# Kernel tuning notes

Measured on AMD Instinct MI355X. Metric: run time of the kernel, lower is better.

## Reference

```python
import jax, jax.numpy as jnp
import numpy as np
import math

D = 1024
H = 16
B = 4
S = 2048


def setup_inputs() -> dict:
    key = jax.random.key(0)
    ks = jax.random.split(key, 11)
    s = 1.0 / math.sqrt(D)
    inp = {
        "queries": jax.random.normal(ks[0], (B, S, D), jnp.float32),
        "keys": jax.random.normal(ks[1], (B, S, D), jnp.float32),
        "values": jax.random.normal(ks[2], (B, S, D), jnp.float32),
        "Wq": jax.random.normal(ks[3], (D, D), jnp.float32) * s,
        "bq": jnp.zeros((D,), jnp.float32),
        "Wk": jax.random.normal(ks[4], (D, D), jnp.float32) * s,
        "bk": jnp.zeros((D,), jnp.float32),
        "Wv": jax.random.normal(ks[5], (D, D), jnp.float32) * s,
        "bv": jnp.zeros((D,), jnp.float32),
        "Wo": jax.random.normal(ks[6], (D, D), jnp.float32) * s,
        "bo": jnp.zeros((D,), jnp.float32),
    }
    return inp


def _split_heads(x):
    # [B, S, D] -> [B, H, S, D//H]
    b, s, d = x.shape
    return x.reshape(b, s, H, d // H).transpose(0, 2, 1, 3)


def reference(queries, keys, values, Wq, bq, Wk, bk, Wv, bv, Wo, bo):
    q = jax.nn.relu(queries @ Wq + bq)
    k = jax.nn.relu(keys @ Wk + bk)
    v = jax.nn.relu(values @ Wv + bv)
    q, k, v = _split_heads(q), _split_heads(k), _split_heads(v)
    dk = q.shape[-1]
    scores = jnp.einsum('bhqd,bhkd->bhqk', q, k) / jnp.sqrt(jnp.float32(dk))
    attn = jax.nn.softmax(scores, axis=-1)
    y = jnp.einsum('bhqk,bhkd->bhqd', attn, v)
    y = y.transpose(0, 2, 1, 3).reshape(queries.shape[0], queries.shape[1], -1)
    return jax.nn.relu(y @ Wo + bo)
```

## Files before the change

### kernel.cpp

```cpp
#include <hip/hip_runtime.h>
#include <hip/hip_bf16.h>
#include <stdint.h>

#define D_MODEL 1024
#define NH 16
#define BB 4
#define SS 2048
#define DKH 64
#define MTOT (BB*SS)

typedef float  f32x4  __attribute__((ext_vector_type(4)));
typedef short  bf16x8 __attribute__((ext_vector_type(8)));
typedef short  bf16x4 __attribute__((ext_vector_type(4)));

static __device__ __forceinline__ unsigned short f2bf(float x) {
    __hip_bfloat16 h = __float2bfloat16(x);
    return *reinterpret_cast<unsigned short*>(&h);
}

static __device__ __forceinline__ void gld_lds16(const void* g, void* l) {
    __builtin_amdgcn_global_load_lds(
        (__attribute__((address_space(1))) const void*)g,
        (__attribute__((address_space(3))) void*)l,
        16, 0, 0);
}

__global__ void cvt_f32_bf16(const float* __restrict__ in,
                             unsigned short* __restrict__ out) {
    const size_t i = ((size_t)blockIdx.x * blockDim.x + threadIdx.x) * 8;
    f32x4 a = *(const f32x4*)(in + i);
    f32x4 b = *(const f32x4*)(in + i + 4);
    bf16x8 o;
#pragma unroll
    for (int j = 0; j < 4; ++j) o[j] = (short)f2bf(a[j]);
#pragma unroll
    for (int j = 0; j < 4; ++j) o[4 + j] = (short)f2bf(b[j]);
    *(bf16x8*)(out + i) = o;
}

__global__ void transpose_cvt(const float* __restrict__ W,
                              unsigned short* __restrict__ WT) {
    __shared__ float tile[32][33];
    const int tx = threadIdx.x;
    const int ty = threadIdx.y;
    const int n0 = blockIdx.x * 32;
    const int k0 = blockIdx.y * 32;
#pragma unroll
    for (int i = 0; i < 32; i += 8)
        tile[ty + i][tx] = W[(size_t)(k0 + ty + i) * D_MODEL + n0 + tx];
    __syncthreads();
#pragma unroll
    for (int i = 0; i < 32; i += 8)
        WT[(size_t)(n0 + ty + i) * D_MODEL + k0 + tx] = f2bf(tile[tx][ty + i]);
}

__global__ __launch_bounds__(256)
void transpose_v(const unsigned short* __restrict__ Vh,
                 unsigned short* __restrict__ Vt) {
    __shared__ unsigned short t[64 * 64];
    const int tid = threadIdx.x;
    const int bh = blockIdx.y;
    const int s0 = blockIdx.x * 64;
    const unsigned short* src = Vh + ((size_t)bh * SS + s0) * DKH;
#pragma unroll
    for (int i = 0; i < 2; ++i) {
        const int v = tid + i * 256;
        const int r = v >> 3;
        const int c = (v & 7) * 8;
        bf16x8 x = *(const bf16x8*)&src[r * DKH + c];
#pragma unroll
        for (int j = 0; j < 8; ++j) {
            const int d = c + j;
            t[d * 64 + (r ^ ((d & 7) << 3))] = (unsigned short)x[j];
        }
    }
    __syncthreads();
    unsigned short* dst = Vt + (size_t)bh * DKH * SS + s0;
#pragma unroll
    for (int i = 0; i < 2; ++i) {
        const int v = tid + i * 256;
        const int d = v >> 3;
        const int ch = (v & 7) * 8;
        bf16x8 o = *(const bf16x8*)&t[d * 64 + ch];
        *(bf16x8*)&dst[(size_t)d * SS + ch] = o;
    }
}

template<int OUT_MODE>
__global__ __launch_bounds__(256)
void gemm_bt_bias_relu(const unsigned short* __restrict__ A,
                       const unsigned short* __restrict__ BT,
                       const float* __restrict__ bias,
                       void* __restrict__ out, float oscale) {
    constexpr int K = 1024, N = 1024, BM = 128, BN = 128, BK = 32;
    __shared__ __align__(16) unsigned short As[BM * BK];
    __shared__ __align__(16) unsigned short Bs[BN * BK];
    const int tid = threadIdx.x;
    const int lane = tid & 63;
    const int w = tid >> 6;
    const int wr = w >> 1, wc = w & 1;
    const int row16 = lane & 15, quad = lane >> 4;
    const int bm = blockIdx.x, bn = blockIdx.y;

    const unsigned short* Ab = A + (size_t)bm * BM * K;
    const unsigned short* Bb = BT + (size_t)bn * BN * K;

    f32x4 acc[4][4] = {};

    for (int k0 = 0; k0 < K; k0 += BK) {
        __syncthreads();
#pragma unroll
        for (int i = 0; i < 2; ++i) {
            const int o = tid * 8 + i * 2048;
            const int r = o >> 5, c = o & 31;
            gld_lds16(Ab + (size_t)r * K + k0 + c, As + o);
            gld_lds16(Bb + (size_t)r * K + k0 + c, Bs + o);
        }
        __syncthreads();
        bf16x8 af[4], bfr[4];
#pragma unroll
        for (int m = 0; m < 4; ++m)
            af[m] = *(const bf16x8*)&As[(wr * 64 + m * 16 + row16) * BK + quad * 8];
#pragma unroll
        for (int n = 0; n < 4; ++n)
            bfr[n] = *(const bf16x8*)&Bs[(wc * 64 + n * 16 + row16) * BK + quad * 8];
        __builtin_amdgcn_s_setprio(1);
#pragma unroll
        for (int m = 0; m < 4; ++m)
#pragma unroll
            for (int n = 0; n < 4; ++n)
                acc[m][n] = __builtin_amdgcn_mfma_f32_16x16x32_bf16(af[m], bfr[n], acc[m][n], 0, 0, 0);
        __builtin_amdgcn_s_setprio(0);
    }

#pragma unroll
    for (int m = 0; m < 4; ++m) {
#pragma unroll
        for (int n = 0; n < 4; ++n) {
            const int gcol = bn * BN + wc * 64 + n * 16 + row16;
            const float bv = bias[gcol];
#pragma unroll
            for (int r = 0; r < 4; ++r) {
                const int grow = bm * BM + wr * 64 + m * 16 + quad * 4 + r;
                float v = fmaxf((acc[m][n][r] + bv) * oscale, 0.0f);
                if (OUT_MODE == 0) {
                    const int b = grow >> 11, s = grow & (SS - 1);
                    const int h = gcol >> 6, d = gcol & (DKH - 1);
                    ((unsigned short*)out)[(((size_t)(b * NH + h) * SS + s) * DKH) + d] = f2bf(v);
                } else {
                    ((float*)out)[(size_t)grow * N + gcol] = v;
                }
            }
        }
    }
}

__global__ __launch_bounds__(256)
void flash_attn(const unsigned short* __restrict__ Qh,
                const unsigned short* __restrict__ Kh,
                const unsigned short* __restrict__ Vt,
                unsigned short* __restrict__ Y) {
    constexpr int KVB = 64;
    __shared__ __align__(16) unsigned short Ks[2 * KVB * 32];
    __shared__ __align__(16) unsigned short Vs[DKH * 64];
    __shared__ __align__(16) unsigned short Ps[4][16 * 64];

    const int tid = threadIdx.x;
    const int lane = tid & 63;
    const int w = tid >> 6;
    const int row16 = lane & 15, quad = lane >> 4;
    const int bh = blockIdx.y;
    const int q0 = blockIdx.x * 64;
    const size_t ho = (size_t)bh * SS * DKH;
    const unsigned short* Qp = Qh + ho;
    const unsigned short* Kp = Kh + ho;
    const unsigned short* Vtp = Vt + ho;
    unsigned short* Pw = &Ps[w][0];

    const int qrow = q0 + w * 16 + row16;
    const bf16x8 qf0 = *(const bf16x8*)&Qp[(size_t)qrow * DKH + quad * 8];
    const bf16x8 qf1 = *(const bf16x8*)&Qp[(size_t)qrow * DKH + 32 + quad * 8];

    const int sw = (row16 & 7) << 3;
    const int xsw0 = (quad * 8) ^ sw;
    const int xsw1 = (32 + quad * 8) ^ sw;

    float m_run[4], l_run[4];
    f32x4 yacc[4] = {};
#pragma unroll
    for (int r = 0; r < 4; ++r) { m_run[r] = -1e30f; l_run[r] = 0.0f; }

    for (int t = 0; t < SS / KVB; ++t) {
        const unsigned short* Kt = Kp + (size_t)t * KVB * DKH;
        __syncthreads();
#pragma unroll
        for (int i = 0; i < 2; ++i) {
            const int o = tid * 8 + i * 2048;
            const int c = o >> 11, rem = o & 2047;
            const int key = rem >> 5, kk = rem & 31;
            gld_lds16(Kt + (size_t)key * DKH + c * 32 + kk, Ks + o);
        }
#pragma unroll
        for (int i = 0; i < 2; ++i) {
            const int c = tid + i * 256;
            const int d = c >> 3, x = (c & 7) * 8;
            gld_lds16(Vtp + (size_t)d * SS + t * KVB + x, Vs + c * 8);
        }
        __syncthreads();

        f32x4 sc[4];
        __builtin_amdgcn_s_setprio(1);
#pragma unroll
        for (int kt = 0; kt < 4; ++kt) {
            bf16x8 kf0 = *(const bf16x8*)&Ks[(kt * 16 + row16) * 32 + quad * 8];
            bf16x8 kf1 = *(const bf16x8*)&Ks[2048 + (kt * 16 + row16) * 32 + quad * 8];
            f32x4 z = {};
            z = __builtin_amdgcn_mfma_f32_16x16x32_bf16(qf0, kf0, z, 0, 0, 0);
            z = __builtin_amdgcn_mfma_f32_16x16x32_bf16(qf1, kf1, z, 0, 0, 0);
            sc[kt] = z;
        }
        __builtin_amdgcn_s_setprio(0);

        float pmax[4];
#pragma unroll
        for (int r = 0; r < 4; ++r) {
            float mx = fmaxf(fmaxf(sc[0][r], sc[1][r]), fmaxf(sc[2][r], sc[3][r]));
#pragma unroll
            for (int off = 1; off < 16; off <<= 1)
                mx = fmaxf(mx, __shfl_xor(mx, off));
            pmax[r] = mx;
        }
        int need = 0;
#pragma unroll
        for (int r = 0; r < 4; ++r) need |= (pmax[r] > m_run[r] + 8.0f);
        if (__any(need)) {
#pragma unroll
            for (int r = 0; r < 4; ++r) {
                const float mnew = fmaxf(m_run[r], pmax[r]);
                const float corr = __builtin_amdgcn_exp2f(m_run[r] - mnew);
                m_run[r] = mnew;
                l_run[r] *= corr;
#pragma unroll
                for (int dt = 0; dt < 4; ++dt) yacc[dt][r] *= corr;
            }
        }
#pragma unroll
        for (int kt = 0; kt < 4; ++kt) {
#pragma unroll
            for (int r = 0; r < 4; ++r) {
                const float p = __builtin_amdgcn_exp2f(sc[kt][r] - m_run[r]);
                l_run[r] += p;
                const int row = quad * 4 + r;
                Pw[row * 64 + ((kt * 16 + row16) ^ ((row & 7) << 3))] = f2bf(p);
            }
        }
        {
            bf16x8 pf0 = *(const bf16x8*)&Pw[row16 * 64 + xsw0];
            bf16x8 pf1 = *(const bf16x8*)&Pw[row16 * 64 + xsw1];
            __builtin_amdgcn_s_setprio(1);
#pragma unroll
            for (int dt = 0; dt < 4; ++dt) {
                bf16x8 vf0 = *(const bf16x8*)&Vs[(dt * 16 + row16) * 64 + xsw0];
                yacc[dt] = __builtin_amdgcn_mfma_f32_16x16x32_bf16(pf0, vf0, yacc[dt], 0, 0, 0);
            }
#pragma unroll
            for (int dt = 0; dt < 4; ++dt) {
                bf16x8 vf1 = *(const bf16x8*)&Vs[(dt * 16 + row16) * 64 + xsw1];
                yacc[dt] = __builtin_amdgcn_mfma_f32_16x16x32_bf16(pf1, vf1, yacc[dt], 0, 0, 0);
            }
            __builtin_amdgcn_s_setprio(0);
        }
    }

    float inv[4];
#pragma unroll
    for (int r = 0; r < 4; ++r) {
        float s = l_run[r];
#pragma unroll
        for (int off = 1; off < 16; off <<= 1)
            s += __shfl_xor(s, off);
        inv[r] = 1.0f / s;
    }
    const int b = bh >> 4, h = bh & 15;
#pragma unroll
    for (int dt = 0; dt < 4; ++dt) {
#pragma unroll
        for (int r = 0; r < 4; ++r) {
            const int row = q0 + w * 16 + quad * 4 + r;
            const int col = h * DKH + dt * 16 + row16;
            Y[(size_t)(b * SS + row) * D_MODEL + col] = f2bf(yacc[dt][r] * inv[r]);
        }
    }
}

extern "C" void kernel_launch(void* const* d_in, const int* in_sizes, int n_in,
                              void* d_out, int out_size, void* d_ws, size_t ws_size,
                              hipStream_t stream) {
    (void)in_sizes; (void)n_in; (void)out_size; (void)ws_size;
    const float* queries = (const float*)d_in[0];
    const float* keys    = (const float*)d_in[1];
    const float* values  = (const float*)d_in[2];
    const float* Wq = (const float*)d_in[3];
    const float* bq = (const float*)d_in[4];
    const float* Wk = (const float*)d_in[5];
    const float* bk = (const float*)d_in[6];
    const float* Wv = (const float*)d_in[7];
    const float* bv = (const float*)d_in[8];
    const float* Wo = (const float*)d_in[9];
    const float* bo = (const float*)d_in[10];

    unsigned short* ws = (unsigned short*)d_ws;
    const size_t SZX = (size_t)MTOT * D_MODEL;
    const size_t SZW = (size_t)D_MODEL * D_MODEL;
    unsigned short* Xq  = ws;
    unsigned short* Xk  = ws + SZX;
    unsigned short* Xv  = ws + 2 * SZX;
    unsigned short* WqT = ws + 3 * SZX;
    unsigned short* WkT = WqT + SZW;
    unsigned short* WvT = WkT + SZW;
    unsigned short* WoT = WvT + SZW;
    unsigned short* Qh  = WoT + SZW;
    unsigned short* Kh  = Qh + SZX;
    unsigned short* Vh  = Kh + SZX;
    unsigned short* Vtr = Xv;
    unsigned short* Yb  = Xq;

    dim3 cblk(256), cgrid((unsigned)(SZX / (256 * 8)));
    cvt_f32_bf16<<<cgrid, cblk, 0, stream>>>(queries, Xq);
    cvt_f32_bf16<<<cgrid, cblk, 0, stream>>>(keys, Xk);
    cvt_f32_bf16<<<cgrid, cblk, 0, stream>>>(values, Xv);

    dim3 tgrid(32, 32), tblk(32, 8);
    transpose_cvt<<<tgrid, tblk, 0, stream>>>(Wq, WqT);
    transpose_cvt<<<tgrid, tblk, 0, stream>>>(Wk, WkT);
    transpose_cvt<<<tgrid, tblk, 0, stream>>>(Wv, WvT);
    transpose_cvt<<<tgrid, tblk, 0, stream>>>(Wo, WoT);

    const float qscale = 0.125f * 1.4426950408889634f;
    dim3 ggrid(MTOT / 128, D_MODEL / 128), gblk(256);
    gemm_bt_bias_relu<0><<<ggrid, gblk, 0, stream>>>(Xq, WqT, bq, Qh, qscale);
    gemm_bt_bias_relu<0><<<ggrid, gblk, 0, stream>>>(Xk, WkT, bk, Kh, 1.0f);
    gemm_bt_bias_relu<0><<<ggrid, gblk, 0, stream>>>(Xv, WvT, bv, Vh, 1.0f);

    dim3 vtgrid(SS / 64, BB * NH);
    transpose_v<<<vtgrid, gblk, 0, stream>>>(Vh, Vtr);

    dim3 agrid(SS / 64, BB * NH), ablk(256);
    flash_attn<<<agrid, ablk, 0, stream>>>(Qh, Kh, Vtr, Yb);

    gemm_bt_bias_relu<1><<<ggrid, gblk, 0, stream>>>(Yb, WoT, bo, d_out, 1.0f);
}
```

Measured before the change: 466.0 us.

## Double-buffer GEMM and attention LDS tiles, merge conversion launches, cheapen rescale check

```diff
diff --git a/kernel.cpp b/kernel.cpp
--- a/kernel.cpp
+++ b/kernel.cpp
@@ -11,7 +11,6 @@
 
 typedef float  f32x4  __attribute__((ext_vector_type(4)));
 typedef short  bf16x8 __attribute__((ext_vector_type(8)));
-typedef short  bf16x4 __attribute__((ext_vector_type(4)));
 
 static __device__ __forceinline__ unsigned short f2bf(float x) {
     __hip_bfloat16 h = __float2bfloat16(x);
@@ -25,8 +24,14 @@
         16, 0, 0);
 }
 
-__global__ void cvt_f32_bf16(const float* __restrict__ in,
-                             unsigned short* __restrict__ out) {
+__global__ void cvt3_f32_bf16(const float* __restrict__ q, const float* __restrict__ k,
+                              const float* __restrict__ v,
+                              unsigned short* __restrict__ oq, unsigned short* __restrict__ ok,
+                              unsigned short* __restrict__ ov) {
+    const float* in; unsigned short* out;
+    if (blockIdx.y == 0)      { in = q; out = oq; }
+    else if (blockIdx.y == 1) { in = k; out = ok; }
+    else                      { in = v; out = ov; }
     const size_t i = ((size_t)blockIdx.x * blockDim.x + threadIdx.x) * 8;
     f32x4 a = *(const f32x4*)(in + i);
     f32x4 b = *(const f32x4*)(in + i + 4);
@@ -38,8 +43,17 @@
     *(bf16x8*)(out + i) = o;
 }
 
-__global__ void transpose_cvt(const float* __restrict__ W,
-                              unsigned short* __restrict__ WT) {
+__global__ void transpose_cvt4(const float* __restrict__ W0, const float* __restrict__ W1,
+                               const float* __restrict__ W2, const float* __restrict__ W3,
+                               unsigned short* __restrict__ T0, unsigned short* __restrict__ T1,
+                               unsigned short* __restrict__ T2, unsigned short* __restrict__ T3) {
+    const float* W; unsigned short* WT;
+    switch (blockIdx.z) {
+        case 0: W = W0; WT = T0; break;
+        case 1: W = W1; WT = T1; break;
+        case 2: W = W2; WT = T2; break;
+        default: W = W3; WT = T3; break;
+    }
     __shared__ float tile[32][33];
     const int tx = threadIdx.x;
     const int ty = threadIdx.y;
@@ -93,8 +107,8 @@
                        const float* __restrict__ bias,
                        void* __restrict__ out, float oscale) {
     constexpr int K = 1024, N = 1024, BM = 128, BN = 128, BK = 32;
-    __shared__ __align__(16) unsigned short As[BM * BK];
-    __shared__ __align__(16) unsigned short Bs[BN * BK];
+    __shared__ __align__(16) unsigned short As[2][BM * BK];
+    __shared__ __align__(16) unsigned short Bs[2][BN * BK];
     const int tid = threadIdx.x;
     const int lane = tid & 63;
     const int w = tid >> 6;
@@ -105,25 +119,34 @@
     const unsigned short* Ab = A + (size_t)bm * BM * K;
     const unsigned short* Bb = BT + (size_t)bn * BN * K;
 
+    const int o0 = tid * 8, o1 = tid * 8 + 2048;
+    const int r0 = o0 >> 5, c0 = o0 & 31;
+    const int r1 = o1 >> 5, c1 = o1 & 31;
+
     f32x4 acc[4][4] = {};
 
-    for (int k0 = 0; k0 < K; k0 += BK) {
-        __syncthreads();
-#pragma unroll
-        for (int i = 0; i < 2; ++i) {
-            const int o = tid * 8 + i * 2048;
-            const int r = o >> 5, c = o & 31;
-            gld_lds16(Ab + (size_t)r * K + k0 + c, As + o);
-            gld_lds16(Bb + (size_t)r * K + k0 + c, Bs + o);
-        }
-        __syncthreads();
+    gld_lds16(Ab + (size_t)r0 * K + c0, &As[0][o0]);
+    gld_lds16(Bb + (size_t)r0 * K + c0, &Bs[0][o0]);
+    gld_lds16(Ab + (size_t)r1 * K + c1, &As[0][o1]);
+    gld_lds16(Bb + (size_t)r1 * K + c1, &Bs[0][o1]);
+    __syncthreads();
+
+    for (int k0 = 0, it = 0; k0 < K; k0 += BK, ++it) {
+        const int cur = it & 1;
+        if (k0 + BK < K) {
+            const int kn = k0 + BK;
+            gld_lds16(Ab + (size_t)r0 * K + kn + c0, &As[cur ^ 1][o0]);
+            gld_lds16(Bb + (size_t)r0 * K + kn + c0, &Bs[cur ^ 1][o0]);
+            gld_lds16(Ab + (size_t)r1 * K + kn + c1, &As[cur ^ 1][o1]);
+            gld_lds16(Bb + (size_t)r1 * K + kn + c1, &Bs[cur ^ 1][o1]);
+        }
         bf16x8 af[4], bfr[4];
 #pragma unroll
         for (int m = 0; m < 4; ++m)
-            af[m] = *(const bf16x8*)&As[(wr * 64 + m * 16 + row16) * BK + quad * 8];
+            af[m] = *(const bf16x8*)&As[cur][(wr * 64 + m * 16 + row16) * BK + quad * 8];
 #pragma unroll
         for (int n = 0; n < 4; ++n)
-            bfr[n] = *(const bf16x8*)&Bs[(wc * 64 + n * 16 + row16) * BK + quad * 8];
+            bfr[n] = *(const bf16x8*)&Bs[cur][(wc * 64 + n * 16 + row16) * BK + quad * 8];
         __builtin_amdgcn_s_setprio(1);
 #pragma unroll
         for (int m = 0; m < 4; ++m)
@@ -131,6 +154,7 @@
             for (int n = 0; n < 4; ++n)
                 acc[m][n] = __builtin_amdgcn_mfma_f32_16x16x32_bf16(af[m], bfr[n], acc[m][n], 0, 0, 0);
         __builtin_amdgcn_s_setprio(0);
+        __syncthreads();
     }
 
 #pragma unroll
@@ -161,8 +185,9 @@
                 const unsigned short* __restrict__ Vt,
                 unsigned short* __restrict__ Y) {
     constexpr int KVB = 64;
-    __shared__ __align__(16) unsigned short Ks[2 * KVB * 32];
-    __shared__ __align__(16) unsigned short Vs[DKH * 64];
+    constexpr int NT = SS / KVB;
+    __shared__ __align__(16) unsigned short Ks[2][KVB * 64];
+    __shared__ __align__(16) unsigned short Vs[2][DKH * 64];
     __shared__ __align__(16) unsigned short Ps[4][16 * 64];
 
     const int tid = threadIdx.x;
@@ -185,35 +210,45 @@
     const int xsw0 = (quad * 8) ^ sw;
     const int xsw1 = (32 + quad * 8) ^ sw;
 
+    const int ko0 = tid * 8,        ko1 = tid * 8 + 2048;
+    const int kr0 = ko0 >> 6,       kr1 = ko1 >> 6;
+    const int ks0 = kr0 * 64 + ((((ko0 >> 3) & 7) ^ (kr0 & 7)) << 3);
+    const int ks1 = kr1 * 64 + ((((ko1 >> 3) & 7) ^ (kr1 & 7)) << 3);
+    const int vd0 = ko0 >> 6, vx0 = ko0 & 63;
+    const int vd1 = ko1 >> 6, vx1 = ko1 & 63;
+
     float m_run[4], l_run[4];
     f32x4 yacc[4] = {};
 #pragma unroll
     for (int r = 0; r < 4; ++r) { m_run[r] = -1e30f; l_run[r] = 0.0f; }
 
-    for (int t = 0; t < SS / KVB; ++t) {
-        const unsigned short* Kt = Kp + (size_t)t * KVB * DKH;
-        __syncthreads();
-#pragma unroll
-        for (int i = 0; i < 2; ++i) {
-            const int o = tid * 8 + i * 2048;
-            const int c = o >> 11, rem = o & 2047;
-            const int key = rem >> 5, kk = rem & 31;
-            gld_lds16(Kt + (size_t)key * DKH + c * 32 + kk, Ks + o);
-        }
-#pragma unroll
-        for (int i = 0; i < 2; ++i) {
-            const int c = tid + i * 256;
-            const int d = c >> 3, x = (c & 7) * 8;
-            gld_lds16(Vtp + (size_t)d * SS + t * KVB + x, Vs + c * 8);
-        }
-        __syncthreads();
+    {
+        const unsigned short* Kt = Kp;
+        gld_lds16(Kt + ks0, &Ks[0][ko0]);
+        gld_lds16(Kt + ks1, &Ks[0][ko1]);
+        gld_lds16(Vtp + (size_t)vd0 * SS + vx0, &Vs[0][ko0]);
+        gld_lds16(Vtp + (size_t)vd1 * SS + vx1, &Vs[0][ko1]);
+    }
+    __syncthreads();
+
+    for (int t = 0; t < NT; ++t) {
+        const int cur = t & 1;
+        if (t + 1 < NT) {
+            const unsigned short* Kt = Kp + (size_t)(t + 1) * KVB * DKH;
+            const int vcol = (t + 1) * KVB;
+            gld_lds16(Kt + ks0, &Ks[cur ^ 1][ko0]);
+            gld_lds16(Kt + ks1, &Ks[cur ^ 1][ko1]);
+            gld_lds16(Vtp + (size_t)vd0 * SS + vcol + vx0, &Vs[cur ^ 1][ko0]);
+            gld_lds16(Vtp + (size_t)vd1 * SS + vcol + vx1, &Vs[cur ^ 1][ko1]);
+        }
 
         f32x4 sc[4];
         __builtin_amdgcn_s_setprio(1);
 #pragma unroll
         for (int kt = 0; kt < 4; ++kt) {
-            bf16x8 kf0 = *(const bf16x8*)&Ks[(kt * 16 + row16) * 32 + quad * 8];
-            bf16x8 kf1 = *(const bf16x8*)&Ks[2048 + (kt * 16 + row16) * 32 + quad * 8];
+            const int key = kt * 16 + row16;
+            bf16x8 kf0 = *(const bf16x8*)&Ks[cur][key * 64 + xsw0];
+            bf16x8 kf1 = *(const bf16x8*)&Ks[cur][key * 64 + xsw1];
             f32x4 z = {};
             z = __builtin_amdgcn_mfma_f32_16x16x32_bf16(qf0, kf0, z, 0, 0, 0);
             z = __builtin_amdgcn_mfma_f32_16x16x32_bf16(qf1, kf1, z, 0, 0, 0);
@@ -221,22 +256,23 @@
         }
         __builtin_amdgcn_s_setprio(0);
 
-        float pmax[4];
-#pragma unroll
-        for (int r = 0; r < 4; ++r) {
-            float mx = fmaxf(fmaxf(sc[0][r], sc[1][r]), fmaxf(sc[2][r], sc[3][r]));
-#pragma unroll
-            for (int off = 1; off < 16; off <<= 1)
-                mx = fmaxf(mx, __shfl_xor(mx, off));
-            pmax[r] = mx;
-        }
-        int need = 0;
-#pragma unroll
-        for (int r = 0; r < 4; ++r) need |= (pmax[r] > m_run[r] + 8.0f);
-        if (__any(need)) {
+        float rl[4];
+#pragma unroll
+        for (int r = 0; r < 4; ++r)
+            rl[r] = fmaxf(fmaxf(sc[0][r], sc[1][r]), fmaxf(sc[2][r], sc[3][r]));
+        float mx = fmaxf(fmaxf(rl[0], rl[1]), fmaxf(rl[2], rl[3]));
+#pragma unroll
+        for (int off = 1; off < 16; off <<= 1)
+            mx = fmaxf(mx, __shfl_xor(mx, off));
+        const float mn = fminf(fminf(m_run[0], m_run[1]), fminf(m_run[2], m_run[3]));
+        if (__any(mx > mn + 8.0f)) {
 #pragma unroll
             for (int r = 0; r < 4; ++r) {
-                const float mnew = fmaxf(m_run[r], pmax[r]);
+                float rm = rl[r];
+#pragma unroll
+                for (int off = 1; off < 16; off <<= 1)
+                    rm = fmaxf(rm, __shfl_xor(rm, off));
+                const float mnew = fmaxf(m_run[r], rm);
                 const float corr = __builtin_amdgcn_exp2f(m_run[r] - mnew);
                 m_run[r] = mnew;
                 l_run[r] *= corr;
@@ -260,16 +296,17 @@
             __builtin_amdgcn_s_setprio(1);
 #pragma unroll
             for (int dt = 0; dt < 4; ++dt) {
-                bf16x8 vf0 = *(const bf16x8*)&Vs[(dt * 16 + row16) * 64 + xsw0];
+                bf16x8 vf0 = *(const bf16x8*)&Vs[cur][(dt * 16 + row16) * 64 + xsw0];
                 yacc[dt] = __builtin_amdgcn_mfma_f32_16x16x32_bf16(pf0, vf0, yacc[dt], 0, 0, 0);
             }
 #pragma unroll
             for (int dt = 0; dt < 4; ++dt) {
-                bf16x8 vf1 = *(const bf16x8*)&Vs[(dt * 16 + row16) * 64 + xsw1];
+                bf16x8 vf1 = *(const bf16x8*)&Vs[cur][(dt * 16 + row16) * 64 + xsw1];
                 yacc[dt] = __builtin_amdgcn_mfma_f32_16x16x32_bf16(pf1, vf1, yacc[dt], 0, 0, 0);
             }
             __builtin_amdgcn_s_setprio(0);
         }
+        __syncthreads();
     }
 
     float inv[4];
@@ -325,16 +362,11 @@
     unsigned short* Vtr = Xv;
     unsigned short* Yb  = Xq;
 
-    dim3 cblk(256), cgrid((unsigned)(SZX / (256 * 8)));
-    cvt_f32_bf16<<<cgrid, cblk, 0, stream>>>(queries, Xq);
-    cvt_f32_bf16<<<cgrid, cblk, 0, stream>>>(keys, Xk);
-    cvt_f32_bf16<<<cgrid, cblk, 0, stream>>>(values, Xv);
-
-    dim3 tgrid(32, 32), tblk(32, 8);
-    transpose_cvt<<<tgrid, tblk, 0, stream>>>(Wq, WqT);
-    transpose_cvt<<<tgrid, tblk, 0, stream>>>(Wk, WkT);
-    transpose_cvt<<<tgrid, tblk, 0, stream>>>(Wv, WvT);
-    transpose_cvt<<<tgrid, tblk, 0, stream>>>(Wo, WoT);
+    dim3 cblk(256), cgrid((unsigned)(SZX / (256 * 8)), 3);
+    cvt3_f32_bf16<<<cgrid, cblk, 0, stream>>>(queries, keys, values, Xq, Xk, Xv);
+
+    dim3 tgrid(32, 32, 4), tblk(32, 8);
+    transpose_cvt4<<<tgrid, tblk, 0, stream>>>(Wq, Wk, Wv, Wo, WqT, WkT, WvT, WoT);
 
     const float qscale = 0.125f * 1.4426950408889634f;
     dim3 ggrid(MTOT / 128, D_MODEL / 128), gblk(256);
```

Measured after the change: 421.1 us. 1.11x faster.
